# Performance work log

Hardware: AMD Instinct MI355X
Metric: run time of the kernel (lower is better)

## Reference

```python
import jax, jax.numpy as jnp
import numpy as np

EPS = 1e-5
N_ENT, N_REL, DIM = 100000, 500, 128
B, K = 2048, 128

def _norm(x):
    # stable L2 norm over last dim, keepdims
    return jnp.sqrt(jnp.sum(x * x, axis=-1, keepdims=True) + 1e-15)

def norm_within_one(x):
    # project onto the open unit ball (Poincare ball, c=1)
    n = _norm(x)
    maxn = 1.0 - EPS
    return jnp.where(n > maxn, x * (maxn / n), x)

def p_log_map(x):
    # log map at the origin: artanh(||x||) * x / ||x||
    n = jnp.clip(_norm(x), EPS, 1.0 - EPS)
    return jnp.arctanh(n) * x / n

def p_exp_map(v):
    # exp map at the origin: tanh(||v||) * v / ||v||
    n = jnp.clip(_norm(v), EPS, None)
    return jnp.tanh(n) * v / n

def p_sum(x, y):
    # Mobius addition (c=1)
    xy = jnp.sum(x * y, axis=-1, keepdims=True)
    x2 = jnp.sum(x * x, axis=-1, keepdims=True)
    y2 = jnp.sum(y * y, axis=-1, keepdims=True)
    num = (1.0 + 2.0 * xy + y2) * x + (1.0 - x2) * y
    den = 1.0 + 2.0 * xy + x2 * y2
    return num / jnp.clip(den, EPS, None)

def calculate_dist(x, y):
    # Poincare distance: arccosh(1 + 2||x-y||^2 / ((1-||x||^2)(1-||y||^2)))
    x2 = jnp.sum(x * x, axis=-1)
    y2 = jnp.sum(y * y, axis=-1)
    d2 = jnp.sum((x - y) ** 2, axis=-1)
    arg = 1.0 + 2.0 * d2 / jnp.clip((1.0 - x2) * (1.0 - y2), EPS, None)
    return jnp.arccosh(jnp.clip(arg, 1.0 + 1e-7, None))

def setup_inputs() -> dict:
    key = jax.random.key(0)
    k1, k2, k3, k4, k5, k6 = jax.random.split(key, 6)
    Eh = 0.001 * jax.random.normal(k1, (N_ENT, DIM), dtype=jnp.float32)
    rvh = 0.001 * jax.random.normal(k2, (N_REL, DIM), dtype=jnp.float32)
    W = jax.random.uniform(k3, (N_REL, DIM), dtype=jnp.float32, minval=-1.0, maxval=1.0)
    bias0 = jnp.zeros((N_ENT,), dtype=jnp.float32)
    bias1 = jnp.zeros((N_ENT,), dtype=jnp.float32)
    head_idx = jax.random.randint(k4, (B, K), 0, N_ENT)
    rel_idx = jax.random.randint(k5, (B, K), 0, N_REL)
    tail_idx = jax.random.randint(k6, (B, K), 0, N_ENT)
    return {"Eh": Eh, "rvh": rvh, "W": W, "bias0": bias0, "bias1": bias1,
            "head_idx": head_idx, "rel_idx": rel_idx, "tail_idx": tail_idx}

def reference(Eh, rvh, W, bias0, bias1, head_idx, rel_idx, tail_idx):
    # gather + project to ball
    h = norm_within_one(Eh[head_idx])          # [B,K,D]
    t = norm_within_one(Eh[tail_idx])          # [B,K,D]
    r = norm_within_one(rvh[rel_idx])          # [B,K,D]
    w = W[rel_idx]                             # [B,K,D]
    # head transform: log map -> diagonal relation scaling -> exp map
    head = norm_within_one(p_exp_map(p_log_map(h) * w))
    # tail transform: Mobius translation by relation vector
    tail = norm_within_one(p_sum(t, r))
    dist = calculate_dist(head, tail)          # [B,K]
    local_bias = bias0[head_idx] + bias1[tail_idx]
    return -dist + local_bias
```

## Files before the change

### kernel.cpp

```cpp
#include <hip/hip_runtime.h>
#include <math.h>


#define EPSF 1e-5f
#define MAXN (1.0f - 1e-5f)

__device__ __forceinline__ float dot4(const float4 a, const float4 b) {
    return a.x * b.x + a.y * b.y + a.z * b.z + a.w * b.w;
}

__device__ __forceinline__ unsigned bfpack(unsigned lo, unsigned hi) {
    unsigned bl = (lo + 0x7FFFu + ((lo >> 16) & 1u)) >> 16;
    unsigned bh = (hi + 0x7FFFu + ((hi >> 16) & 1u)) & 0xFFFF0000u;
    return (bl & 0xFFFFu) | bh;
}

__global__ __launch_bounds__(256) void cvt_bf16_kernel(
    const uint4* __restrict__ src, uint4* __restrict__ dst, int ngroups)
{
    int i = blockIdx.x * 256 + threadIdx.x;
    if (i >= ngroups) return;
    uint4 a = src[2 * i];
    uint4 b = src[2 * i + 1];
    uint4 o;
    o.x = bfpack(a.x, a.y);
    o.y = bfpack(a.z, a.w);
    o.z = bfpack(b.x, b.y);
    o.w = bfpack(b.z, b.w);
    dst[i] = o;
}

__device__ __forceinline__ float bflo(unsigned u) { return __uint_as_float(u << 16); }
__device__ __forceinline__ float bfhi(unsigned u) { return __uint_as_float(u & 0xFFFF0000u); }

__device__ __forceinline__ void gload_lds16(const void* g, void* l) {
    typedef const __attribute__((address_space(1))) unsigned int GU;
    typedef __attribute__((address_space(3))) unsigned int LU;
    __builtin_amdgcn_global_load_lds((GU*)g, (LU*)l, 16, 0, 0);
}

__global__ __launch_bounds__(256) void poincare_score_lds_kernel(
    const char* __restrict__ Ehb, const float* __restrict__ rvh,
    const float* __restrict__ W, const float* __restrict__ bias0,
    const float* __restrict__ bias1, const int* __restrict__ head_idx,
    const int* __restrict__ rel_idx, const int* __restrict__ tail_idx,
    float* __restrict__ out, int total)
{
    __shared__ uint4 lds[4][512];

    const int lane  = threadIdx.x & 63;
    const int wave  = threadIdx.x >> 6;
    const int sub   = lane & 3;
    const int e     = blockIdx.x * 64 + wave * 16 + (lane >> 2);
    const int ec    = (e < total) ? e : (total - 1);

    const int hi = head_idx[ec];
    const int ri = rel_idx[ec];
    const int ti = tail_idx[ec];

    uint4* __restrict__ ldsw = lds[wave];

    const char* hg = Ehb + ((size_t)(unsigned)hi << 8) + (sub << 4);
    const char* tg = Ehb + ((size_t)(unsigned)ti << 8) + (sub << 4);

#pragma unroll
    for (int k = 0; k < 4; ++k)
        gload_lds16(hg + k * 64, (void*)(ldsw + k * 64));
#pragma unroll
    for (int k = 0; k < 4; ++k)
        gload_lds16(tg + k * 64, (void*)(ldsw + 256 + k * 64));

    const float4* __restrict__ rrow =
        reinterpret_cast<const float4*>(rvh) + (size_t)ri * 32 + sub * 2;
    const float4* __restrict__ wrow =
        reinterpret_cast<const float4*>(W)   + (size_t)ri * 32 + sub * 2;

    asm volatile("s_waitcnt vmcnt(0)" ::: "memory");
    __builtin_amdgcn_sched_barrier(0);

    float H2 = 0.f, T2 = 0.f, R2 = 0.f, TR = 0.f;
    float HW2 = 0.f, HWT = 0.f, HWR = 0.f;

#pragma unroll
    for (int k = 0; k < 4; ++k) {
        uint4 hq = ldsw[k * 64 + lane];
        uint4 tq = ldsw[256 + k * 64 + lane];
        float4 r0 = rrow[k * 8], r1 = rrow[k * 8 + 1];
        float4 w0 = wrow[k * 8], w1 = wrow[k * 8 + 1];

        float4 ha = make_float4(bflo(hq.x), bfhi(hq.x), bflo(hq.y), bfhi(hq.y));
        float4 hb = make_float4(bflo(hq.z), bfhi(hq.z), bflo(hq.w), bfhi(hq.w));
        float4 ta = make_float4(bflo(tq.x), bfhi(tq.x), bflo(tq.y), bfhi(tq.y));
        float4 tb = make_float4(bflo(tq.z), bfhi(tq.z), bflo(tq.w), bfhi(tq.w));

        float4 hwa, hwb;
        hwa.x = ha.x * w0.x; hwa.y = ha.y * w0.y; hwa.z = ha.z * w0.z; hwa.w = ha.w * w0.w;
        hwb.x = hb.x * w1.x; hwb.y = hb.y * w1.y; hwb.z = hb.z * w1.z; hwb.w = hb.w * w1.w;

        H2  += dot4(ha, ha)   + dot4(hb, hb);
        T2  += dot4(ta, ta)   + dot4(tb, tb);
        R2  += dot4(r0, r0)   + dot4(r1, r1);
        TR  += dot4(ta, r0)   + dot4(tb, r1);
        HW2 += dot4(hwa, hwa) + dot4(hwb, hwb);
        HWT += dot4(hwa, ta)  + dot4(hwb, tb);
        HWR += dot4(hwa, r0)  + dot4(hwb, r1);
    }

#pragma unroll
    for (int m = 1; m <= 2; m <<= 1) {
        H2  += __shfl_xor(H2,  m);
        T2  += __shfl_xor(T2,  m);
        R2  += __shfl_xor(R2,  m);
        TR  += __shfl_xor(TR,  m);
        HW2 += __shfl_xor(HW2, m);
        HWT += __shfl_xor(HWT, m);
        HWR += __shfl_xor(HWR, m);
    }

    float nh = sqrtf(H2 + 1e-15f);
    float sh = (nh > MAXN) ? (MAXN / nh) : 1.0f;
    float h2 = H2 * sh * sh;

    float nt = sqrtf(T2 + 1e-15f);
    float st = (nt > MAXN) ? (MAXN / nt) : 1.0f;
    float t2 = T2 * st * st;

    float nr = sqrtf(R2 + 1e-15f);
    float sr = (nr > MAXN) ? (MAXN / nr) : 1.0f;
    float r2 = R2 * sr * sr;

    float xy = TR * st * sr;

    float nl = sqrtf(h2 + 1e-15f);
    nl = fminf(fmaxf(nl, EPSF), MAXN);
    float lf = 0.5f * logf((1.0f + nl) / (1.0f - nl)) / nl;
    float a0 = lf * sh;
    float v2 = a0 * a0 * HW2;

    float nv = fmaxf(sqrtf(v2 + 1e-15f), EPSF);
    float ef = tanhf(nv) / nv;
    float b0 = ef * a0;
    float hd2 = b0 * b0 * HW2;

    float nhd = sqrtf(hd2 + 1e-15f);
    float shd = (nhd > MAXN) ? (MAXN / nhd) : 1.0f;
    float b = b0 * shd;
    hd2 = b * b * HW2;

    float ct  = 1.0f + 2.0f * xy + r2;
    float cr  = 1.0f - t2;
    float den = fmaxf(1.0f + 2.0f * xy + t2 * r2, EPSF);
    float id  = 1.0f / den;
    float p = id * ct * st;
    float q = id * cr * sr;
    float tl2 = p * p * T2 + 2.0f * p * q * TR + q * q * R2;

    float ntl = sqrtf(tl2 + 1e-15f);
    float stl = (ntl > MAXN) ? (MAXN / ntl) : 1.0f;
    p *= stl; q *= stl;
    tl2 = tl2 * stl * stl;

    float hdtl = b * (p * HWT + q * HWR);
    float d2   = hd2 + tl2 - 2.0f * hdtl;
    float dn   = fmaxf((1.0f - hd2) * (1.0f - tl2), EPSF);
    float arg  = fmaxf(1.0f + 2.0f * d2 / dn, 1.0f + 1e-7f);
    float dist = acoshf(arg);

    if (sub == 0 && e < total) {
        out[e] = bias0[hi] + bias1[ti] - dist;
    }
}

__global__ __launch_bounds__(256) void poincare_score_f32_kernel(
    const float* __restrict__ Eh, const float* __restrict__ rvh,
    const float* __restrict__ W, const float* __restrict__ bias0,
    const float* __restrict__ bias1, const int* __restrict__ head_idx,
    const int* __restrict__ rel_idx, const int* __restrict__ tail_idx,
    float* __restrict__ out, int total)
{
    const int tid   = threadIdx.x;
    const int lane4 = tid & 3;
    const int e     = blockIdx.x * 64 + (tid >> 2);
    if (e >= total) return;

    const int hi = head_idx[e];
    const int ri = rel_idx[e];
    const int ti = tail_idx[e];

    const float4* __restrict__ Eh4  = reinterpret_cast<const float4*>(Eh);
    const float4* __restrict__ rvh4 = reinterpret_cast<const float4*>(rvh);
    const float4* __restrict__ W4   = reinterpret_cast<const float4*>(W);

    const float4* __restrict__ hrow = Eh4  + (size_t)hi * 32 + lane4;
    const float4* __restrict__ trow = Eh4  + (size_t)ti * 32 + lane4;
    const float4* __restrict__ rrow = rvh4 + (size_t)ri * 32 + lane4;
    const float4* __restrict__ wrow = W4   + (size_t)ri * 32 + lane4;

    float H2 = 0.f, T2 = 0.f, R2 = 0.f, TR = 0.f;
    float HW2 = 0.f, HWT = 0.f, HWR = 0.f;
#pragma unroll
    for (int j = 0; j < 8; ++j) {
        float4 h = hrow[j * 4];
        float4 t = trow[j * 4];
        float4 r = rrow[j * 4];
        float4 w = wrow[j * 4];
        float4 hw;
        hw.x = h.x * w.x; hw.y = h.y * w.y; hw.z = h.z * w.z; hw.w = h.w * w.w;
        H2  += dot4(h, h);
        T2  += dot4(t, t);
        R2  += dot4(r, r);
        TR  += dot4(t, r);
        HW2 += dot4(hw, hw);
        HWT += dot4(hw, t);
        HWR += dot4(hw, r);
    }
#pragma unroll
    for (int m = 1; m <= 2; m <<= 1) {
        H2  += __shfl_xor(H2,  m);
        T2  += __shfl_xor(T2,  m);
        R2  += __shfl_xor(R2,  m);
        TR  += __shfl_xor(TR,  m);
        HW2 += __shfl_xor(HW2, m);
        HWT += __shfl_xor(HWT, m);
        HWR += __shfl_xor(HWR, m);
    }

    float nh = sqrtf(H2 + 1e-15f);
    float sh = (nh > MAXN) ? (MAXN / nh) : 1.0f;
    float h2 = H2 * sh * sh;
    float nt = sqrtf(T2 + 1e-15f);
    float st = (nt > MAXN) ? (MAXN / nt) : 1.0f;
    float t2 = T2 * st * st;
    float nr = sqrtf(R2 + 1e-15f);
    float sr = (nr > MAXN) ? (MAXN / nr) : 1.0f;
    float r2 = R2 * sr * sr;
    float xy = TR * st * sr;

    float nl = sqrtf(h2 + 1e-15f);
    nl = fminf(fmaxf(nl, EPSF), MAXN);
    float lf = 0.5f * logf((1.0f + nl) / (1.0f - nl)) / nl;
    float a0 = lf * sh;
    float v2 = a0 * a0 * HW2;
    float nv = fmaxf(sqrtf(v2 + 1e-15f), EPSF);
    float ef = tanhf(nv) / nv;
    float b0 = ef * a0;
    float hd2 = b0 * b0 * HW2;
    float nhd = sqrtf(hd2 + 1e-15f);
    float shd = (nhd > MAXN) ? (MAXN / nhd) : 1.0f;
    float b = b0 * shd;
    hd2 = b * b * HW2;

    float ct  = 1.0f + 2.0f * xy + r2;
    float cr  = 1.0f - t2;
    float den = fmaxf(1.0f + 2.0f * xy + t2 * r2, EPSF);
    float id  = 1.0f / den;
    float p = id * ct * st;
    float q = id * cr * sr;
    float tl2 = p * p * T2 + 2.0f * p * q * TR + q * q * R2;
    float ntl = sqrtf(tl2 + 1e-15f);
    float stl = (ntl > MAXN) ? (MAXN / ntl) : 1.0f;
    p *= stl; q *= stl;
    tl2 = tl2 * stl * stl;

    float hdtl = b * (p * HWT + q * HWR);
    float d2   = hd2 + tl2 - 2.0f * hdtl;
    float dn   = fmaxf((1.0f - hd2) * (1.0f - tl2), EPSF);
    float arg  = fmaxf(1.0f + 2.0f * d2 / dn, 1.0f + 1e-7f);
    float dist = acoshf(arg);

    if (lane4 == 0) {
        out[e] = bias0[hi] + bias1[ti] - dist;
    }
}

extern "C" void kernel_launch(void* const* d_in, const int* in_sizes, int n_in,
                              void* d_out, int out_size, void* d_ws, size_t ws_size,
                              hipStream_t stream) {
    const float* Eh       = (const float*)d_in[0];
    const float* rvh      = (const float*)d_in[1];
    const float* W        = (const float*)d_in[2];
    const float* bias0    = (const float*)d_in[3];
    const float* bias1    = (const float*)d_in[4];
    const int*   head_idx = (const int*)d_in[5];
    const int*   rel_idx  = (const int*)d_in[6];
    const int*   tail_idx = (const int*)d_in[7];
    float* out = (float*)d_out;

    const int total  = in_sizes[5];
    const int blocks = (total + 63) / 64;

    const int n_eh = in_sizes[0];
    const size_t need = (size_t)n_eh * 2;

    if (ws_size >= need && (n_eh & 7) == 0) {
        const int ngroups = n_eh / 8;
        const int cblocks = (ngroups + 255) / 256;
        cvt_bf16_kernel<<<cblocks, 256, 0, stream>>>(
            (const uint4*)Eh, (uint4*)d_ws, ngroups);
        poincare_score_lds_kernel<<<blocks, 256, 0, stream>>>(
            (const char*)d_ws, rvh, W, bias0, bias1,
            head_idx, rel_idx, tail_idx, out, total);
    } else {
        poincare_score_f32_kernel<<<blocks, 256, 0, stream>>>(
            Eh, rvh, W, bias0, bias1, head_idx, rel_idx, tail_idx, out, total);
    }
}
```

Before: 50.77 us.

## Convert scoring kernel to persistent waves with double-buffered LDS row prefetch

The one-shot LDS gather kernel becomes a persistent grid-stride kernel. Each wave loops over groups of 8 elements, with 8 lanes per element instead of 4. While it computes the current group, it prefetches the next group's bf16 head and tail rows into a second LDS buffer, and it loads indices two iterations ahead. The aim is to hide gather latency behind the transcendental math. The cost is a manual vmcnt accounting that has to stay in step with the issued loads, and a fixed grid of 1280 blocks.

```diff
diff --git a/kernel.cpp b/kernel.cpp
--- a/kernel.cpp
+++ b/kernel.cpp
@@ -6,7 +6,7 @@
 #define MAXN (1.0f - 1e-5f)
 
 __device__ __forceinline__ float dot4(const float4 a, const float4 b) {
-    return a.x * b.x + a.y * b.y + a.z * b.z + a.w * b.w;
+    return a.x*b.x + a.y*b.y + a.z*b.z + a.w*b.w;
 }
 
 __device__ __forceinline__ unsigned bfpack(unsigned lo, unsigned hi) {
@@ -20,18 +20,15 @@
 {
     int i = blockIdx.x * 256 + threadIdx.x;
     if (i >= ngroups) return;
-    uint4 a = src[2 * i];
-    uint4 b = src[2 * i + 1];
+    uint4 a = src[2*i], b = src[2*i+1];
     uint4 o;
-    o.x = bfpack(a.x, a.y);
-    o.y = bfpack(a.z, a.w);
-    o.z = bfpack(b.x, b.y);
-    o.w = bfpack(b.z, b.w);
+    o.x = bfpack(a.x, a.y); o.y = bfpack(a.z, a.w);
+    o.z = bfpack(b.x, b.y); o.w = bfpack(b.z, b.w);
     dst[i] = o;
 }
 
-__device__ __forceinline__ float bflo(unsigned u) { return __uint_as_float(u << 16); }
-__device__ __forceinline__ float bfhi(unsigned u) { return __uint_as_float(u & 0xFFFF0000u); }
+__device__ __forceinline__ float bflo(unsigned u){ return __uint_as_float(u<<16); }
+__device__ __forceinline__ float bfhi(unsigned u){ return __uint_as_float(u&0xFFFF0000u); }
 
 __device__ __forceinline__ void gload_lds16(const void* g, void* l) {
     typedef const __attribute__((address_space(1))) unsigned int GU;
@@ -39,135 +36,152 @@
     __builtin_amdgcn_global_load_lds((GU*)g, (LU*)l, 16, 0, 0);
 }
 
-__global__ __launch_bounds__(256) void poincare_score_lds_kernel(
+__global__ __launch_bounds__(256, 4) void poincare_score_pipe_kernel(
     const char* __restrict__ Ehb, const float* __restrict__ rvh,
     const float* __restrict__ W, const float* __restrict__ bias0,
     const float* __restrict__ bias1, const int* __restrict__ head_idx,
     const int* __restrict__ rel_idx, const int* __restrict__ tail_idx,
-    float* __restrict__ out, int total)
+    float* __restrict__ out, int total, int nb, int stride)
 {
-    __shared__ uint4 lds[4][512];
-
-    const int lane  = threadIdx.x & 63;
-    const int wave  = threadIdx.x >> 6;
-    const int sub   = lane & 3;
-    const int e     = blockIdx.x * 64 + wave * 16 + (lane >> 2);
-    const int ec    = (e < total) ? e : (total - 1);
-
-    const int hi = head_idx[ec];
-    const int ri = rel_idx[ec];
-    const int ti = tail_idx[ec];
-
-    uint4* __restrict__ ldsw = lds[wave];
-
-    const char* hg = Ehb + ((size_t)(unsigned)hi << 8) + (sub << 4);
-    const char* tg = Ehb + ((size_t)(unsigned)ti << 8) + (sub << 4);
-
+    __shared__ uint4 lds[4][2][256];
+
+    const int lane = threadIdx.x & 63;
+    const int wave = threadIdx.x >> 6;
+    const int sub  = lane & 7;
+    const int eg   = lane >> 3;
+    const int wid  = blockIdx.x * 4 + wave;
+    if (wid >= nb) return;
+
+    const int tmax = total - 1;
+
+    int b = wid;
+    int e0 = b*8 + eg; e0 = e0 > tmax ? tmax : e0;
+    int hi0 = head_idx[e0], ri0 = rel_idx[e0], ti0 = tail_idx[e0];
+    {
+        const char* hg = Ehb + ((size_t)(unsigned)hi0 << 8) + (sub << 4);
+        const char* tg = Ehb + ((size_t)(unsigned)ti0 << 8) + (sub << 4);
+        uint4* bp = &lds[wave][0][0];
+        gload_lds16(hg,       bp);         gload_lds16(hg + 128, bp + 64);
+        gload_lds16(tg,       bp + 128);   gload_lds16(tg + 128, bp + 192);
+    }
+    int b1 = b + stride; b1 = b1 >= nb ? nb - 1 : b1;
+    int e1 = b1*8 + eg; e1 = e1 > tmax ? tmax : e1;
+    int hi1 = head_idx[e1], ri1 = rel_idx[e1], ti1 = tail_idx[e1];
+
+    int pb = 0;
+    for (; b < nb; b += stride) {
+        const bool has_next = (b + stride) < nb;
+        if (has_next) {
+            const char* hg = Ehb + ((size_t)(unsigned)hi1 << 8) + (sub << 4);
+            const char* tg = Ehb + ((size_t)(unsigned)ti1 << 8) + (sub << 4);
+            uint4* bp = &lds[wave][pb ^ 1][0];
+            gload_lds16(hg,       bp);         gload_lds16(hg + 128, bp + 64);
+            gload_lds16(tg,       bp + 128);   gload_lds16(tg + 128, bp + 192);
+        }
+        int b2 = b + 2*stride; b2 = b2 >= nb ? nb - 1 : b2;
+        int e2 = b2*8 + eg; e2 = e2 > tmax ? tmax : e2;
+        int hi2 = head_idx[e2], ri2 = rel_idx[e2], ti2 = tail_idx[e2];
+
+        if (has_next) asm volatile("s_waitcnt vmcnt(7)" ::: "memory");
+        else          asm volatile("s_waitcnt vmcnt(0)" ::: "memory");
+        __builtin_amdgcn_sched_barrier(0);
+
+        const uint4* __restrict__ cur = &lds[wave][pb][0];
+        const float4* __restrict__ rrow = (const float4*)rvh + (size_t)ri0*32 + sub*2;
+        const float4* __restrict__ wrow = (const float4*)W   + (size_t)ri0*32 + sub*2;
+
+        float H2=0.f,T2=0.f,R2=0.f,TR=0.f,HW2=0.f,HWT=0.f,HWR=0.f;
 #pragma unroll
-    for (int k = 0; k < 4; ++k)
-        gload_lds16(hg + k * 64, (void*)(ldsw + k * 64));
+        for (int c = 0; c < 2; ++c) {
+            uint4 hq = cur[c*64 + lane];
+            uint4 tq = cur[128 + c*64 + lane];
+            float4 r0 = rrow[c*16], r1 = rrow[c*16 + 1];
+            float4 w0 = wrow[c*16], w1 = wrow[c*16 + 1];
+
+            float4 ha = make_float4(bflo(hq.x),bfhi(hq.x),bflo(hq.y),bfhi(hq.y));
+            float4 hb = make_float4(bflo(hq.z),bfhi(hq.z),bflo(hq.w),bfhi(hq.w));
+            float4 ta = make_float4(bflo(tq.x),bfhi(tq.x),bflo(tq.y),bfhi(tq.y));
+            float4 tb = make_float4(bflo(tq.z),bfhi(tq.z),bflo(tq.w),bfhi(tq.w));
+
+            float4 hwa, hwb;
+            hwa.x=ha.x*w0.x; hwa.y=ha.y*w0.y; hwa.z=ha.z*w0.z; hwa.w=ha.w*w0.w;
+            hwb.x=hb.x*w1.x; hwb.y=hb.y*w1.y; hwb.z=hb.z*w1.z; hwb.w=hb.w*w1.w;
+
+            H2  += dot4(ha,ha)   + dot4(hb,hb);
+            T2  += dot4(ta,ta)   + dot4(tb,tb);
+            R2  += dot4(r0,r0)   + dot4(r1,r1);
+            TR  += dot4(ta,r0)   + dot4(tb,r1);
+            HW2 += dot4(hwa,hwa) + dot4(hwb,hwb);
+            HWT += dot4(hwa,ta)  + dot4(hwb,tb);
+            HWR += dot4(hwa,r0)  + dot4(hwb,r1);
+        }
 #pragma unroll
-    for (int k = 0; k < 4; ++k)
-        gload_lds16(tg + k * 64, (void*)(ldsw + 256 + k * 64));
-
-    const float4* __restrict__ rrow =
-        reinterpret_cast<const float4*>(rvh) + (size_t)ri * 32 + sub * 2;
-    const float4* __restrict__ wrow =
-        reinterpret_cast<const float4*>(W)   + (size_t)ri * 32 + sub * 2;
-
-    asm volatile("s_waitcnt vmcnt(0)" ::: "memory");
-    __builtin_amdgcn_sched_barrier(0);
-
-    float H2 = 0.f, T2 = 0.f, R2 = 0.f, TR = 0.f;
-    float HW2 = 0.f, HWT = 0.f, HWR = 0.f;
-
-#pragma unroll
-    for (int k = 0; k < 4; ++k) {
-        uint4 hq = ldsw[k * 64 + lane];
-        uint4 tq = ldsw[256 + k * 64 + lane];
-        float4 r0 = rrow[k * 8], r1 = rrow[k * 8 + 1];
-        float4 w0 = wrow[k * 8], w1 = wrow[k * 8 + 1];
-
-        float4 ha = make_float4(bflo(hq.x), bfhi(hq.x), bflo(hq.y), bfhi(hq.y));
-        float4 hb = make_float4(bflo(hq.z), bfhi(hq.z), bflo(hq.w), bfhi(hq.w));
-        float4 ta = make_float4(bflo(tq.x), bfhi(tq.x), bflo(tq.y), bfhi(tq.y));
-        float4 tb = make_float4(bflo(tq.z), bfhi(tq.z), bflo(tq.w), bfhi(tq.w));
-
-        float4 hwa, hwb;
-        hwa.x = ha.x * w0.x; hwa.y = ha.y * w0.y; hwa.z = ha.z * w0.z; hwa.w = ha.w * w0.w;
-        hwb.x = hb.x * w1.x; hwb.y = hb.y * w1.y; hwb.z = hb.z * w1.z; hwb.w = hb.w * w1.w;
-
-        H2  += dot4(ha, ha)   + dot4(hb, hb);
-        T2  += dot4(ta, ta)   + dot4(tb, tb);
-        R2  += dot4(r0, r0)   + dot4(r1, r1);
-        TR  += dot4(ta, r0)   + dot4(tb, r1);
-        HW2 += dot4(hwa, hwa) + dot4(hwb, hwb);
-        HWT += dot4(hwa, ta)  + dot4(hwb, tb);
-        HWR += dot4(hwa, r0)  + dot4(hwb, r1);
-    }
-
-#pragma unroll
-    for (int m = 1; m <= 2; m <<= 1) {
-        H2  += __shfl_xor(H2,  m);
-        T2  += __shfl_xor(T2,  m);
-        R2  += __shfl_xor(R2,  m);
-        TR  += __shfl_xor(TR,  m);
-        HW2 += __shfl_xor(HW2, m);
-        HWT += __shfl_xor(HWT, m);
-        HWR += __shfl_xor(HWR, m);
-    }
-
-    float nh = sqrtf(H2 + 1e-15f);
-    float sh = (nh > MAXN) ? (MAXN / nh) : 1.0f;
-    float h2 = H2 * sh * sh;
-
-    float nt = sqrtf(T2 + 1e-15f);
-    float st = (nt > MAXN) ? (MAXN / nt) : 1.0f;
-    float t2 = T2 * st * st;
-
-    float nr = sqrtf(R2 + 1e-15f);
-    float sr = (nr > MAXN) ? (MAXN / nr) : 1.0f;
-    float r2 = R2 * sr * sr;
-
-    float xy = TR * st * sr;
-
-    float nl = sqrtf(h2 + 1e-15f);
-    nl = fminf(fmaxf(nl, EPSF), MAXN);
-    float lf = 0.5f * logf((1.0f + nl) / (1.0f - nl)) / nl;
-    float a0 = lf * sh;
-    float v2 = a0 * a0 * HW2;
-
-    float nv = fmaxf(sqrtf(v2 + 1e-15f), EPSF);
-    float ef = tanhf(nv) / nv;
-    float b0 = ef * a0;
-    float hd2 = b0 * b0 * HW2;
-
-    float nhd = sqrtf(hd2 + 1e-15f);
-    float shd = (nhd > MAXN) ? (MAXN / nhd) : 1.0f;
-    float b = b0 * shd;
-    hd2 = b * b * HW2;
-
-    float ct  = 1.0f + 2.0f * xy + r2;
-    float cr  = 1.0f - t2;
-    float den = fmaxf(1.0f + 2.0f * xy + t2 * r2, EPSF);
-    float id  = 1.0f / den;
-    float p = id * ct * st;
-    float q = id * cr * sr;
-    float tl2 = p * p * T2 + 2.0f * p * q * TR + q * q * R2;
-
-    float ntl = sqrtf(tl2 + 1e-15f);
-    float stl = (ntl > MAXN) ? (MAXN / ntl) : 1.0f;
-    p *= stl; q *= stl;
-    tl2 = tl2 * stl * stl;
-
-    float hdtl = b * (p * HWT + q * HWR);
-    float d2   = hd2 + tl2 - 2.0f * hdtl;
-    float dn   = fmaxf((1.0f - hd2) * (1.0f - tl2), EPSF);
-    float arg  = fmaxf(1.0f + 2.0f * d2 / dn, 1.0f + 1e-7f);
-    float dist = acoshf(arg);
-
-    if (sub == 0 && e < total) {
-        out[e] = bias0[hi] + bias1[ti] - dist;
+        for (int m = 1; m <= 4; m <<= 1) {
+            H2  += __shfl_xor(H2,  m);
+            T2  += __shfl_xor(T2,  m);
+            R2  += __shfl_xor(R2,  m);
+            TR  += __shfl_xor(TR,  m);
+            HW2 += __shfl_xor(HW2, m);
+            HWT += __shfl_xor(HWT, m);
+            HWR += __shfl_xor(HWR, m);
+        }
+
+        float nh = sqrtf(H2 + 1e-15f);
+        float sh = (nh > MAXN) ? (MAXN / nh) : 1.0f;
+        float h2 = H2 * sh * sh;
+
+        float nt = sqrtf(T2 + 1e-15f);
+        float st = (nt > MAXN) ? (MAXN / nt) : 1.0f;
+        float t2 = T2 * st * st;
+
+        float nr = sqrtf(R2 + 1e-15f);
+        float sr = (nr > MAXN) ? (MAXN / nr) : 1.0f;
+        float r2 = R2 * sr * sr;
+
+        float xy = TR * st * sr;
+
+        float nl = sqrtf(h2 + 1e-15f);
+        nl = fminf(fmaxf(nl, EPSF), MAXN);
+        float lf = 0.5f * logf((1.0f + nl) / (1.0f - nl)) / nl;
+        float a0 = lf * sh;
+        float v2 = a0 * a0 * HW2;
+
+        float nv = fmaxf(sqrtf(v2 + 1e-15f), EPSF);
+        float ef = tanhf(nv) / nv;
+        float b0 = ef * a0;
+        float hd2 = b0 * b0 * HW2;
+
+        float nhd = sqrtf(hd2 + 1e-15f);
+        float shd = (nhd > MAXN) ? (MAXN / nhd) : 1.0f;
+        float bb = b0 * shd;
+        hd2 = bb * bb * HW2;
+
+        float ct  = 1.0f + 2.0f * xy + r2;
+        float cr  = 1.0f - t2;
+        float den = fmaxf(1.0f + 2.0f * xy + t2 * r2, EPSF);
+        float id  = 1.0f / den;
+        float p = id * ct * st;
+        float q = id * cr * sr;
+        float tl2 = p*p*T2 + 2.0f*p*q*TR + q*q*R2;
+
+        float ntl = sqrtf(tl2 + 1e-15f);
+        float stl = (ntl > MAXN) ? (MAXN / ntl) : 1.0f;
+        p *= stl; q *= stl;
+        tl2 = tl2 * stl * stl;
+
+        float hdtl = bb * (p * HWT + q * HWR);
+        float d2   = hd2 + tl2 - 2.0f * hdtl;
+        float dn   = fmaxf((1.0f - hd2) * (1.0f - tl2), EPSF);
+        float arg  = fmaxf(1.0f + 2.0f * d2 / dn, 1.0f + 1e-7f);
+        float dist = acoshf(arg);
+
+        int e = b*8 + eg;
+        if (sub == 0 && e < total)
+            out[e] = bias0[hi0] + bias1[ti0] - dist;
+
+        hi0 = hi1; ri0 = ri1; ti0 = ti1;
+        hi1 = hi2; ri1 = ri2; ti1 = ti2;
+        pb ^= 1;
     }
 }
 
@@ -286,10 +300,8 @@
     const int*   tail_idx = (const int*)d_in[7];
     float* out = (float*)d_out;
 
-    const int total  = in_sizes[5];
-    const int blocks = (total + 63) / 64;
-
-    const int n_eh = in_sizes[0];
+    const int total = in_sizes[5];
+    const int n_eh  = in_sizes[0];
     const size_t need = (size_t)n_eh * 2;
 
     if (ws_size >= need && (n_eh & 7) == 0) {
@@ -297,10 +309,15 @@
         const int cblocks = (ngroups + 255) / 256;
         cvt_bf16_kernel<<<cblocks, 256, 0, stream>>>(
             (const uint4*)Eh, (uint4*)d_ws, ngroups);
-        poincare_score_lds_kernel<<<blocks, 256, 0, stream>>>(
+
+        const int nb      = (total + 7) / 8;
+        const int pblocks = 1280;
+        const int stride  = pblocks * 4;
+        poincare_score_pipe_kernel<<<pblocks, 256, 0, stream>>>(
             (const char*)d_ws, rvh, W, bias0, bias1,
-            head_idx, rel_idx, tail_idx, out, total);
+            head_idx, rel_idx, tail_idx, out, total, nb, stride);
     } else {
+        const int blocks = (total + 63) / 64;
         poincare_score_f32_kernel<<<blocks, 256, 0, stream>>>(
             Eh, rvh, W, bias0, bias1, head_idx, rel_idx, tail_idx, out, total);
     }
```

Result: slower. 62.49 us (+23.1%).
